# Kernel tuning notes

Measured on AMD Instinct MI355X. Metric: run time of the kernel, lower is better.

## Reference

```python
import jax, jax.numpy as jnp
import numpy as np


def setup_inputs() -> dict:
    key = jax.random.key(0)
    kx, kw = jax.random.split(key)
    A_MAX = 16  # activations in [0, 2**A_bits - 1] = [0, 15]
    W_MAX = 15  # torch.randint(0, 2**W_bits - 1) -> [0, 14]
    x = jax.random.randint(kx, (32, 256, 56, 56), 0, A_MAX, dtype=jnp.int32)
    weight = jax.random.randint(kw, (256, 256, 3, 3), 0, W_MAX, dtype=jnp.int32)
    return {"x": x, "weight": weight}


def reference(x, weight):
    # Low-bit quantized conv2d: direct_conv2d(x.int(), w.int(), stride=1) with the
    # module's crop for (k=3, padding=1) is equivalent to a conv with padding=1.
    # Max accumulator value = 15*14*9*256 < 2**24, so fp32 accumulation is exact.
    xf = x.astype(jnp.float32)
    wf = weight.astype(jnp.float32)
    y = jax.lax.conv_general_dilated(
        xf, wf,
        window_strides=(1, 1),
        padding=((1, 1), (1, 1)),
        dimension_numbers=("NCHW", "OIHW", "NCHW"),
    )
    return y.astype(jnp.int32)  # [32, 256, 56, 56]
```

## Files before the change

### kernel.cpp

```cpp
#include <hip/hip_runtime.h>

typedef int v4i  __attribute__((ext_vector_type(4)));
typedef int v16i __attribute__((ext_vector_type(16)));

#define N_IMG   32
#define C_IN    256
#define HWDIM   56
#define HW2     3136
#define OUT_TOT 25690112
#define OUT_NSTR 802816

#define PXB     272
#define PPI     3364
#define XP_IMG  915008
#define XP_SLACK 4096
#define WP_CB2STR 73728
#define WP_BYTES  589824ull

#define S_TILE  64
#define TILES_PER_IMG 49
#define WIN_B   50048

__global__ void dc_x_to_nhwc(const int* __restrict__ x, unsigned int* __restrict__ x8,
                             int n0) {
    __shared__ unsigned int lds[64 * 65];
    const int t = threadIdx.x;
    const int w = t & 63, q = t >> 6;
    const int nl = blockIdx.x / HWDIM, h = blockIdx.x % HWDIM;

    if (w < HWDIM) {
        const int* xb = x + (size_t)(n0 + nl) * OUT_NSTR + h * HWDIM + w;
        #pragma unroll
        for (int it = 0; it < 16; ++it) {
            const int cg4 = q * 16 + it;
            const int ci0 = cg4 * 4;
            unsigned v  =  ((unsigned)xb[(ci0 + 0) * HW2] & 0xff);
            v |= ((unsigned)xb[(ci0 + 1) * HW2] & 0xff) << 8;
            v |= ((unsigned)xb[(ci0 + 2) * HW2] & 0xff) << 16;
            v |= ((unsigned)xb[(ci0 + 3) * HW2] & 0xff) << 24;
            lds[w * 65 + cg4] = v;
        }
    }
    __syncthreads();
    unsigned int* ob = x8 + (size_t)nl * (PPI * (PXB / 4)) + ((h + 1) * 58 + 1) * (PXB / 4);
    #pragma unroll
    for (int it = 0; it < 14; ++it) {
        const int f = it * 256 + t;
        const int w2 = f >> 6, cg = f & 63;
        if (w2 < HWDIM) ob[w2 * (PXB / 4) + cg] = lds[w2 * 65 + cg];
    }
}

__global__ void dc_halo(unsigned int* __restrict__ x8) {
    const int nl = blockIdx.x;
    const int t = threadIdx.x;
    if (t < 228) {
        int h, w;
        if (t < 58)       { h = 0;        w = t; }
        else if (t < 116) { h = 57;       w = t - 58; }
        else if (t < 172) { h = t - 115;  w = 0; }
        else              { h = t - 171;  w = 57; }
        unsigned int* p = x8 + ((size_t)nl * PPI + h * 58 + w) * (PXB / 4);
        #pragma unroll
        for (int i = 0; i < PXB / 4; ++i) p[i] = 0;
    }
}

__global__ void dc_pack_w(const int* __restrict__ wt, unsigned int* __restrict__ wp) {
    const int tid = blockIdx.x * 256 + threadIdx.x;
    const int jq = tid & 3;
    const int l  = (tid >> 2) & 63;
    const int kb = (tid >> 8) & 7;
    const int r  = tid >> 11;
    const int t  = r % 9;
    const int cb2 = r / 9;
    const int co  = cb2 * 32 + (l & 31);
    const int ci0 = kb * 32 + (l >> 5) * 16 + jq * 4;
    const int kh = t / 3, kw = t - kh * 3;
    unsigned v = 0;
    #pragma unroll
    for (int k = 0; k < 4; ++k) {
        unsigned b = (unsigned)wt[((co * C_IN + ci0 + k) * 3 + kh) * 3 + kw];
        v |= (b & 0xff) << (8 * k);
    }
    wp[tid] = v;
}

__device__ __forceinline__ void gll16(const char* g, char* l) {
    __builtin_amdgcn_global_load_lds(
        (const __attribute__((address_space(1))) unsigned int*)g,
        (__attribute__((address_space(3))) unsigned int*)l, 16, 0, 0);
}

__global__ __launch_bounds__(256, 3) void dc_mfma(const char* __restrict__ x8,
                                                  const char* __restrict__ wp,
                                                  int* __restrict__ out, int nwg) {
    extern __shared__ __align__(16) char xs[];

    const int bid = blockIdx.x;
    const int q = nwg >> 3, r = nwg & 7;
    const int xcd = bid & 7, bidx = bid >> 3;
    const int wgid = (xcd < r ? xcd * (q + 1) : r * (q + 1) + (xcd - r) * q) + bidx;

    const int nl = wgid / TILES_PER_IMG, st = wgid - nl * TILES_PER_IMG;

    const int tid = threadIdx.x;
    const int l = tid & 63, wid = tid >> 6;
    const int lane31 = l & 31, hi = l >> 5;

    const int hw0 = st * S_TILE;
    const int h0 = hw0 / HWDIM, w0 = hw0 - h0 * HWDIM;
    const int p0 = h0 * 58 + w0;
    const char* gsrc = x8 + (size_t)nl * XP_IMG + (size_t)p0 * PXB;

    #pragma unroll
    for (int c = 0; c < 13; ++c) {
        const int off = (c * 256 + tid) * 16;
        if (off < WIN_B) gll16(gsrc + off, xs + off);
    }

    int breg[2], outb[2];
    #pragma unroll
    for (int ni = 0; ni < 2; ++ni) {
        const int hw = hw0 + ni * 32 + lane31;
        const int h = hw / HWDIM, w = hw - h * HWDIM;
        const int p = (h + 1) * 58 + (w + 1);
        breg[ni] = (p - p0) * PXB + hi * 16 - 16048;
        outb[ni] = nl * OUT_NSTR + hw;
    }

    const char* wb0 = wp + (wid * 2) * WP_CB2STR + l * 16;
    const char* wb1 = wb0 + WP_CB2STR;

    const int xoffp[9] = {
        16048 - 59 * PXB, 16048 - 58 * PXB, 16048 - 57 * PXB,
        16048 - 1 * PXB,  16048,            16048 + 1 * PXB,
        16048 + 57 * PXB, 16048 + 58 * PXB, 16048 + 59 * PXB
    };

    v16i acc[2][2] = {};
    v4i wa[8][2];
    v4i xb[2][2];

    #pragma unroll
    for (int d = 0; d < 6; ++d) {
        wa[d][0] = *(const v4i*)(wb0 + d * 1024);
        wa[d][1] = *(const v4i*)(wb1 + d * 1024);
    }

    __syncthreads();

    xb[0][0] = *(const v4i*)(xs + breg[0] + xoffp[0]);
    xb[0][1] = *(const v4i*)(xs + breg[1] + xoffp[0]);

    #pragma unroll
    for (int j = 0; j < 72; ++j) {
        const int jc = j & 7;
        const int pc = j & 1;
        if (j + 6 < 72) {
            const int jn = (j + 6) & 7;
            wa[jn][0] = *(const v4i*)(wb0 + (j + 6) * 1024);
            wa[jn][1] = *(const v4i*)(wb1 + (j + 6) * 1024);
        }
        if (j + 1 < 72) {
            const int t1 = (j + 1) >> 3, kb1 = (j + 1) & 7;
            const int xo = xoffp[t1] + kb1 * 32;
            xb[pc ^ 1][0] = *(const v4i*)(xs + breg[0] + xo);
            xb[pc ^ 1][1] = *(const v4i*)(xs + breg[1] + xo);
        }
        __builtin_amdgcn_s_setprio(1);
        acc[0][0] = __builtin_amdgcn_mfma_i32_32x32x32_i8(wa[jc][0], xb[pc][0], acc[0][0], 0, 0, 0);
        acc[0][1] = __builtin_amdgcn_mfma_i32_32x32x32_i8(wa[jc][0], xb[pc][1], acc[0][1], 0, 0, 0);
        acc[1][0] = __builtin_amdgcn_mfma_i32_32x32x32_i8(wa[jc][1], xb[pc][0], acc[1][0], 0, 0, 0);
        acc[1][1] = __builtin_amdgcn_mfma_i32_32x32x32_i8(wa[jc][1], xb[pc][1], acc[1][1], 0, 0, 0);
        __builtin_amdgcn_s_setprio(0);
    }

    #pragma unroll
    for (int mi = 0; mi < 2; ++mi) {
        #pragma unroll
        for (int ni = 0; ni < 2; ++ni) {
            const v16i c = acc[mi][ni];
            int* ob = out + outb[ni] + (wid * 64 + mi * 32 + 4 * hi) * HW2;
            #pragma unroll
            for (int rr = 0; rr < 16; ++rr) {
                __builtin_nontemporal_store(c[rr], ob + ((rr & 3) + 8 * (rr >> 2)) * HW2);
            }
        }
    }
}

__global__ void dc_naive(const int* __restrict__ x, const int* __restrict__ wt,
                         int* __restrict__ out) {
    const int idx = blockIdx.x * 256 + threadIdx.x;
    if (idx >= OUT_TOT) return;
    const int w = idx % HWDIM;
    const int h = (idx / HWDIM) % HWDIM;
    const int co = (idx / HW2) & 255;
    const int n = idx / OUT_NSTR;
    const int* xn = x + n * OUT_NSTR;
    const int* wo = wt + co * (C_IN * 9);
    int acc = 0;
    for (int ci = 0; ci < C_IN; ++ci) {
        const int* xc = xn + ci * HW2;
        const int* wc = wo + ci * 9;
        #pragma unroll
        for (int kh = 0; kh < 3; ++kh) {
            const int hh = h + kh - 1;
            if ((unsigned)hh >= HWDIM) continue;
            #pragma unroll
            for (int kw = 0; kw < 3; ++kw) {
                const int ww = w + kw - 1;
                if ((unsigned)ww >= HWDIM) continue;
                acc += xc[hh * HWDIM + ww] * wc[kh * 3 + kw];
            }
        }
    }
    out[idx] = acc;
}

extern "C" void kernel_launch(void* const* d_in, const int* in_sizes, int n_in,
                              void* d_out, int out_size, void* d_ws, size_t ws_size,
                              hipStream_t stream) {
    const int* x  = (const int*)d_in[0];
    const int* wt = (const int*)d_in[1];
    int* out = (int*)d_out;

    int chunk = 0;
    const int cand[4] = {32, 16, 8, 4};
    for (int i = 0; i < 4; ++i) {
        if ((size_t)cand[i] * XP_IMG + XP_SLACK + WP_BYTES <= ws_size) { chunk = cand[i]; break; }
    }

    if (chunk > 0) {
        char* x8 = (char*)d_ws;
        const size_t x8_bytes = (size_t)chunk * XP_IMG + XP_SLACK;
        unsigned int* wp = (unsigned int*)(x8 + x8_bytes);
        hipLaunchKernelGGL(dc_halo, dim3(chunk), dim3(256), 0, stream, (unsigned int*)x8);
        hipLaunchKernelGGL(dc_pack_w, dim3(576), dim3(256), 0, stream, wt, wp);
        for (int n0 = 0; n0 < N_IMG; n0 += chunk) {
            hipLaunchKernelGGL(dc_x_to_nhwc, dim3(chunk * HWDIM), dim3(256), 0, stream,
                               x, (unsigned int*)x8, n0);
            const int nwg = chunk * TILES_PER_IMG;
            hipLaunchKernelGGL(dc_mfma, dim3(nwg), dim3(256), WIN_B, stream,
                               (const char*)x8, (const char*)wp,
                               out + (size_t)n0 * OUT_NSTR, nwg);
        }
        return;
    }

    hipLaunchKernelGGL(dc_naive, dim3((OUT_TOT + 255) / 256), dim3(256), 0, stream,
                       x, wt, out);
}
```

Measured before the change: 92.94 us.

## Stream weights through LDS ring and XOR-swizzle activation layout

Weights are no longer loaded from global memory straight into registers by each wave. The workgroup now streams them into a 4-slot LDS ring with global_load_lds, which lets the four waves share each weight fetch, and a barrier runs every k-step. The activation pixel stride drops from a padded 272 bytes to 256, and an XOR swizzle in the NHWC pack avoids LDS bank conflicts. The weight pack order changes to match the ring, and occupancy is lowered to 2 blocks per CU because LDS use grows. The cost is 72 barriers per tile and lower occupancy, traded for less redundant global weight traffic and fewer registers.

```diff
diff --git a/kernel.cpp b/kernel.cpp
--- a/kernel.cpp
+++ b/kernel.cpp
@@ -10,29 +10,30 @@
 #define OUT_TOT 25690112
 #define OUT_NSTR 802816
 
-#define PXB     272
+#define PXB     256
 #define PPI     3364
-#define XP_IMG  915008
+#define XP_IMG  861184
 #define XP_SLACK 4096
-#define WP_CB2STR 73728
 #define WP_BYTES  589824ull
 
 #define S_TILE  64
 #define TILES_PER_IMG 49
-#define WIN_B   50048
+#define WIN_B   47104
+#define WRING_B 32768
+#define LDSB    (WIN_B + WRING_B)
 
 __global__ void dc_x_to_nhwc(const int* __restrict__ x, unsigned int* __restrict__ x8,
                              int n0) {
     __shared__ unsigned int lds[64 * 65];
     const int t = threadIdx.x;
-    const int w = t & 63, q = t >> 6;
+    const int w = t & 63, qq = t >> 6;
     const int nl = blockIdx.x / HWDIM, h = blockIdx.x % HWDIM;
 
     if (w < HWDIM) {
         const int* xb = x + (size_t)(n0 + nl) * OUT_NSTR + h * HWDIM + w;
         #pragma unroll
         for (int it = 0; it < 16; ++it) {
-            const int cg4 = q * 16 + it;
+            const int cg4 = qq * 16 + it;
             const int ci0 = cg4 * 4;
             unsigned v  =  ((unsigned)xb[(ci0 + 0) * HW2] & 0xff);
             v |= ((unsigned)xb[(ci0 + 1) * HW2] & 0xff) << 8;
@@ -42,12 +43,16 @@
         }
     }
     __syncthreads();
-    unsigned int* ob = x8 + (size_t)nl * (PPI * (PXB / 4)) + ((h + 1) * 58 + 1) * (PXB / 4);
+    unsigned int* ob = x8 + (size_t)nl * (XP_IMG / 4) + ((h + 1) * 58 + 1) * (PXB / 4);
     #pragma unroll
     for (int it = 0; it < 14; ++it) {
         const int f = it * 256 + t;
         const int w2 = f >> 6, cg = f & 63;
-        if (w2 < HWDIM) ob[w2 * (PXB / 4) + cg] = lds[w2 * 65 + cg];
+        if (w2 < HWDIM) {
+            const int key = ((h + 1) * 58 + w2 + 1) & 15;
+            const int cg2 = (((cg >> 2) ^ key) << 2) | (cg & 3);
+            ob[w2 * (PXB / 4) + cg2] = lds[w2 * 65 + cg];
+        }
     }
 }
 
@@ -83,7 +88,8 @@
         unsigned b = (unsigned)wt[((co * C_IN + ci0 + k) * 3 + kh) * 3 + kw];
         v |= (b & 0xff) << (8 * k);
     }
-    wp[tid] = v;
+    const int dst = (((t * 8 + kb) * 8 + cb2) * 64 + l) * 4 + jq;
+    wp[dst] = v;
 }
 
 __device__ __forceinline__ void gll16(const char* g, char* l) {
@@ -92,10 +98,11 @@
         (__attribute__((address_space(3))) unsigned int*)l, 16, 0, 0);
 }
 
-__global__ __launch_bounds__(256, 3) void dc_mfma(const char* __restrict__ x8,
+__global__ __launch_bounds__(256, 2) void dc_mfma(const char* __restrict__ x8,
                                                   const char* __restrict__ wp,
                                                   int* __restrict__ out, int nwg) {
     extern __shared__ __align__(16) char xs[];
+    char* wring = xs + WIN_B;
 
     const int bid = blockIdx.x;
     const int q = nwg >> 3, r = nwg & 7;
@@ -114,66 +121,74 @@
     const char* gsrc = x8 + (size_t)nl * XP_IMG + (size_t)p0 * PXB;
 
     #pragma unroll
-    for (int c = 0; c < 13; ++c) {
+    for (int c = 0; c < 12; ++c) {
         const int off = (c * 256 + tid) * 16;
         if (off < WIN_B) gll16(gsrc + off, xs + off);
     }
 
-    int breg[2], outb[2];
+    const char* wsrc = wp + tid * 16;
+    char* wdst = wring + tid * 16;
+    gll16(wsrc,            wdst);
+    gll16(wsrc + 4096,     wdst + 4096);
+    gll16(wsrc + 8192,     wdst + 8192);
+    gll16(wsrc + 12288,    wdst + 12288);
+
+    int rbase[2], Pb[2], outb[2];
     #pragma unroll
     for (int ni = 0; ni < 2; ++ni) {
         const int hw = hw0 + ni * 32 + lane31;
         const int h = hw / HWDIM, w = hw - h * HWDIM;
-        const int p = (h + 1) * 58 + (w + 1);
-        breg[ni] = (p - p0) * PXB + hi * 16 - 16048;
+        Pb[ni] = (h + 1) * 58 + (w + 1);
+        rbase[ni] = Pb[ni] - p0;
         outb[ni] = nl * OUT_NSTR + hw;
     }
 
-    const char* wb0 = wp + (wid * 2) * WP_CB2STR + l * 16;
-    const char* wb1 = wb0 + WP_CB2STR;
-
-    const int xoffp[9] = {
-        16048 - 59 * PXB, 16048 - 58 * PXB, 16048 - 57 * PXB,
-        16048 - 1 * PXB,  16048,            16048 + 1 * PXB,
-        16048 + 57 * PXB, 16048 + 58 * PXB, 16048 + 59 * PXB
-    };
-
+    asm volatile("s_waitcnt vmcnt(2)" ::: "memory");
+    __builtin_amdgcn_sched_barrier(0);
+    __builtin_amdgcn_s_barrier();
+    __builtin_amdgcn_sched_barrier(0);
+
+    const int dtap[9] = {-59, -58, -57, -1, 0, 1, 57, 58, 59};
     v16i acc[2][2] = {};
-    v4i wa[8][2];
-    v4i xb[2][2];
-
-    #pragma unroll
-    for (int d = 0; d < 6; ++d) {
-        wa[d][0] = *(const v4i*)(wb0 + d * 1024);
-        wa[d][1] = *(const v4i*)(wb1 + d * 1024);
-    }
-
-    __syncthreads();
-
-    xb[0][0] = *(const v4i*)(xs + breg[0] + xoffp[0]);
-    xb[0][1] = *(const v4i*)(xs + breg[1] + xoffp[0]);
-
-    #pragma unroll
-    for (int j = 0; j < 72; ++j) {
-        const int jc = j & 7;
-        const int pc = j & 1;
-        if (j + 6 < 72) {
-            const int jn = (j + 6) & 7;
-            wa[jn][0] = *(const v4i*)(wb0 + (j + 6) * 1024);
-            wa[jn][1] = *(const v4i*)(wb1 + (j + 6) * 1024);
-        }
-        if (j + 1 < 72) {
-            const int t1 = (j + 1) >> 3, kb1 = (j + 1) & 7;
-            const int xo = xoffp[t1] + kb1 * 32;
-            xb[pc ^ 1][0] = *(const v4i*)(xs + breg[0] + xo);
-            xb[pc ^ 1][1] = *(const v4i*)(xs + breg[1] + xo);
-        }
-        __builtin_amdgcn_s_setprio(1);
-        acc[0][0] = __builtin_amdgcn_mfma_i32_32x32x32_i8(wa[jc][0], xb[pc][0], acc[0][0], 0, 0, 0);
-        acc[0][1] = __builtin_amdgcn_mfma_i32_32x32x32_i8(wa[jc][0], xb[pc][1], acc[0][1], 0, 0, 0);
-        acc[1][0] = __builtin_amdgcn_mfma_i32_32x32x32_i8(wa[jc][1], xb[pc][0], acc[1][0], 0, 0, 0);
-        acc[1][1] = __builtin_amdgcn_mfma_i32_32x32x32_i8(wa[jc][1], xb[pc][1], acc[1][1], 0, 0, 0);
-        __builtin_amdgcn_s_setprio(0);
+
+    #pragma unroll
+    for (int t = 0; t < 9; ++t) {
+        int xbase[2], xkey[2];
+        #pragma unroll
+        for (int ni = 0; ni < 2; ++ni) {
+            const int rt = rbase[ni] + dtap[t];
+            const int key = (Pb[ni] + dtap[t]) & 15;
+            xbase[ni] = rt * PXB + ((hi ^ (key & 1)) << 4);
+            xkey[ni] = (key >> 1) & 7;
+        }
+        #pragma unroll
+        for (int kb = 0; kb < 8; ++kb) {
+            const int j = t * 8 + kb;
+            if (j + 2 < 72) {
+                const int pn = j + 2, slot = pn & 3;
+                gll16(wsrc + pn * 8192,        wdst + slot * 8192);
+                gll16(wsrc + pn * 8192 + 4096, wdst + slot * 8192 + 4096);
+            }
+            if (j < 70)       asm volatile("s_waitcnt vmcnt(4)" ::: "memory");
+            else if (j == 70) asm volatile("s_waitcnt vmcnt(2)" ::: "memory");
+            else              asm volatile("s_waitcnt vmcnt(0)" ::: "memory");
+            __builtin_amdgcn_sched_barrier(0);
+            __builtin_amdgcn_s_barrier();
+            __builtin_amdgcn_sched_barrier(0);
+
+            const char* wslot = wring + (j & 3) * 8192 + l * 16;
+            const v4i wf0 = *(const v4i*)(wslot + (wid * 2 + 0) * 1024);
+            const v4i wf1 = *(const v4i*)(wslot + (wid * 2 + 1) * 1024);
+            const v4i xf0 = *(const v4i*)(xs + xbase[0] + ((kb ^ xkey[0]) << 5));
+            const v4i xf1 = *(const v4i*)(xs + xbase[1] + ((kb ^ xkey[1]) << 5));
+
+            __builtin_amdgcn_s_setprio(1);
+            acc[0][0] = __builtin_amdgcn_mfma_i32_32x32x32_i8(wf0, xf0, acc[0][0], 0, 0, 0);
+            acc[0][1] = __builtin_amdgcn_mfma_i32_32x32x32_i8(wf0, xf1, acc[0][1], 0, 0, 0);
+            acc[1][0] = __builtin_amdgcn_mfma_i32_32x32x32_i8(wf1, xf0, acc[1][0], 0, 0, 0);
+            acc[1][1] = __builtin_amdgcn_mfma_i32_32x32x32_i8(wf1, xf1, acc[1][1], 0, 0, 0);
+            __builtin_amdgcn_s_setprio(0);
+        }
     }
 
     #pragma unroll
@@ -242,7 +257,7 @@
             hipLaunchKernelGGL(dc_x_to_nhwc, dim3(chunk * HWDIM), dim3(256), 0, stream,
                                x, (unsigned int*)x8, n0);
             const int nwg = chunk * TILES_PER_IMG;
-            hipLaunchKernelGGL(dc_mfma, dim3(nwg), dim3(256), WIN_B, stream,
+            hipLaunchKernelGGL(dc_mfma, dim3(nwg), dim3(256), LDSB, stream,
                                (const char*)x8, (const char*)wp,
                                out + (size_t)n0 * OUT_NSTR, nwg);
         }
```

Measured after the change: 111.3 us. +19.7%, slower.

## Split output channels across eight waves with smaller per-wave MFMA tile

Applied to the files above, without the earlier changes.

Doubles the workgroup to 512 threads, so each of eight waves computes 32 output channels by 64 pixels instead of 64 by 64. The per-wave register footprint shrinks (two accumulators, three weight buffers, no activation double-buffer), which is meant to raise occupancy and share the LDS input window across more waves. The cost is half the MFMA reuse per LDS activation read, so LDS traffic per MFMA doubles, and the activation loads are no longer prefetched a step ahead.

```diff
diff --git a/kernel.cpp b/kernel.cpp
--- a/kernel.cpp
+++ b/kernel.cpp
@@ -92,7 +92,7 @@
         (__attribute__((address_space(3))) unsigned int*)l, 16, 0, 0);
 }
 
-__global__ __launch_bounds__(256, 3) void dc_mfma(const char* __restrict__ x8,
+__global__ __launch_bounds__(512, 6) void dc_mfma(const char* __restrict__ x8,
                                                   const char* __restrict__ wp,
                                                   int* __restrict__ out, int nwg) {
     extern __shared__ __align__(16) char xs[];
@@ -114,8 +114,8 @@
     const char* gsrc = x8 + (size_t)nl * XP_IMG + (size_t)p0 * PXB;
 
     #pragma unroll
-    for (int c = 0; c < 13; ++c) {
-        const int off = (c * 256 + tid) * 16;
+    for (int c = 0; c < 7; ++c) {
+        const int off = (c * 512 + tid) * 16;
         if (off < WIN_B) gll16(gsrc + off, xs + off);
     }
 
@@ -129,8 +129,7 @@
         outb[ni] = nl * OUT_NSTR + hw;
     }
 
-    const char* wb0 = wp + (wid * 2) * WP_CB2STR + l * 16;
-    const char* wb1 = wb0 + WP_CB2STR;
+    const char* wb = wp + wid * WP_CB2STR + l * 16;
 
     const int xoffp[9] = {
         16048 - 59 * PXB, 16048 - 58 * PXB, 16048 - 57 * PXB,
@@ -138,54 +137,38 @@
         16048 + 57 * PXB, 16048 + 58 * PXB, 16048 + 59 * PXB
     };
 
-    v16i acc[2][2] = {};
-    v4i wa[8][2];
-    v4i xb[2][2];
-
-    #pragma unroll
-    for (int d = 0; d < 6; ++d) {
-        wa[d][0] = *(const v4i*)(wb0 + d * 1024);
-        wa[d][1] = *(const v4i*)(wb1 + d * 1024);
-    }
-
     __syncthreads();
 
-    xb[0][0] = *(const v4i*)(xs + breg[0] + xoffp[0]);
-    xb[0][1] = *(const v4i*)(xs + breg[1] + xoffp[0]);
+    v16i acc[2] = {};
+    v4i wa[3];
+
+    wa[0] = *(const v4i*)(wb);
+    wa[1] = *(const v4i*)(wb + 1024);
 
     #pragma unroll
     for (int j = 0; j < 72; ++j) {
-        const int jc = j & 7;
-        const int pc = j & 1;
-        if (j + 6 < 72) {
-            const int jn = (j + 6) & 7;
-            wa[jn][0] = *(const v4i*)(wb0 + (j + 6) * 1024);
-            wa[jn][1] = *(const v4i*)(wb1 + (j + 6) * 1024);
-        }
-        if (j + 1 < 72) {
-            const int t1 = (j + 1) >> 3, kb1 = (j + 1) & 7;
-            const int xo = xoffp[t1] + kb1 * 32;
-            xb[pc ^ 1][0] = *(const v4i*)(xs + breg[0] + xo);
-            xb[pc ^ 1][1] = *(const v4i*)(xs + breg[1] + xo);
-        }
+        const int jc = j % 3;
+        if (j + 2 < 72)
+            wa[(j + 2) % 3] = *(const v4i*)(wb + (j + 2) * 1024);
+
+        const int t = j >> 3, kb = j & 7;
+        const int xo = xoffp[t] + kb * 32;
+        const v4i xf0 = *(const v4i*)(xs + breg[0] + xo);
+        const v4i xf1 = *(const v4i*)(xs + breg[1] + xo);
+
         __builtin_amdgcn_s_setprio(1);
-        acc[0][0] = __builtin_amdgcn_mfma_i32_32x32x32_i8(wa[jc][0], xb[pc][0], acc[0][0], 0, 0, 0);
-        acc[0][1] = __builtin_amdgcn_mfma_i32_32x32x32_i8(wa[jc][0], xb[pc][1], acc[0][1], 0, 0, 0);
-        acc[1][0] = __builtin_amdgcn_mfma_i32_32x32x32_i8(wa[jc][1], xb[pc][0], acc[1][0], 0, 0, 0);
-        acc[1][1] = __builtin_amdgcn_mfma_i32_32x32x32_i8(wa[jc][1], xb[pc][1], acc[1][1], 0, 0, 0);
+        acc[0] = __builtin_amdgcn_mfma_i32_32x32x32_i8(wa[jc], xf0, acc[0], 0, 0, 0);
+        acc[1] = __builtin_amdgcn_mfma_i32_32x32x32_i8(wa[jc], xf1, acc[1], 0, 0, 0);
         __builtin_amdgcn_s_setprio(0);
     }
 
     #pragma unroll
-    for (int mi = 0; mi < 2; ++mi) {
-        #pragma unroll
-        for (int ni = 0; ni < 2; ++ni) {
-            const v16i c = acc[mi][ni];
-            int* ob = out + outb[ni] + (wid * 64 + mi * 32 + 4 * hi) * HW2;
-            #pragma unroll
-            for (int rr = 0; rr < 16; ++rr) {
-                __builtin_nontemporal_store(c[rr], ob + ((rr & 3) + 8 * (rr >> 2)) * HW2);
-            }
+    for (int ni = 0; ni < 2; ++ni) {
+        const v16i c = acc[ni];
+        int* ob = out + outb[ni] + (wid * 32 + 4 * hi) * HW2;
+        #pragma unroll
+        for (int rr = 0; rr < 16; ++rr) {
+            __builtin_nontemporal_store(c[rr], ob + ((rr & 3) + 8 * (rr >> 2)) * HW2);
         }
     }
 }
@@ -242,7 +225,7 @@
             hipLaunchKernelGGL(dc_x_to_nhwc, dim3(chunk * HWDIM), dim3(256), 0, stream,
                                x, (unsigned int*)x8, n0);
             const int nwg = chunk * TILES_PER_IMG;
-            hipLaunchKernelGGL(dc_mfma, dim3(nwg), dim3(256), WIN_B, stream,
+            hipLaunchKernelGGL(dc_mfma, dim3(nwg), dim3(512), WIN_B, stream,
                                (const char*)x8, (const char*)wp,
                                out + (size_t)n0 * OUT_NSTR, nwg);
         }
```

New measurement: 99.14 us. 6.7% more time.
